# Kernel optimization log

Hardware: AMD Instinct MI355X
Metric: run time of the kernel (lower is better)

The kernel has to match this reference:

```python
import jax, jax.numpy as jnp
import numpy as np

H = 16       # query heads
KV = 4       # key/value heads
HD = 256     # head dim
ROPE_THETA = 10000.0
EPS = 1e-6


def _rms_norm(x, w):
    # Gemma RMSNorm over last dim: x / rms * (1 + w), computed in fp32
    xf = x.astype(jnp.float32)
    var = jnp.mean(xf * xf, axis=-1, keepdims=True)
    out = xf * jax.lax.rsqrt(var + EPS) * (1.0 + w.astype(jnp.float32))
    return out.astype(x.dtype)


def _rope_cos_sin(position_ids):
    # cos/sin tables of shape [S, HD]
    inv_freq = 1.0 / (ROPE_THETA ** (jnp.arange(0, HD, 2, dtype=jnp.float32) / HD))
    ang = position_ids.astype(jnp.float32)[:, None] * inv_freq[None, :]  # [S, HD/2]
    emb = jnp.concatenate([ang, ang], axis=-1)                           # [S, HD]
    return jnp.cos(emb), jnp.sin(emb)


def _rotate_half(x):
    x1, x2 = jnp.split(x, 2, axis=-1)
    return jnp.concatenate([-x2, x1], axis=-1)


def _apply_rope(x, cos, sin):
    # x: [B, h, S, HD]; cos/sin: [S, HD] -> broadcast over batch and heads
    c = cos[None, None, :, :]
    s = sin[None, None, :, :]
    return (x * c + _rotate_half(x) * s).astype(x.dtype)


def setup_inputs() -> dict:
    key = jax.random.key(0)
    ks = jax.random.split(key, 8)
    B, S, D = 2, 2048, 2048
    inp = {
        "hidden_states": jax.random.normal(ks[0], (B, S, D), jnp.float32),
        "Wq": jax.random.normal(ks[1], (D, H * HD), jnp.float32) * 0.02,
        "Wk": jax.random.normal(ks[2], (D, KV * HD), jnp.float32) * 0.02,
        "Wv": jax.random.normal(ks[3], (D, KV * HD), jnp.float32) * 0.02,
        "Wo": jax.random.normal(ks[4], (H * HD, D), jnp.float32) * 0.02,
        "q_norm_w": jnp.zeros((HD,), jnp.float32),
        "k_norm_w": jnp.zeros((HD,), jnp.float32),
        "position_ids": jnp.arange(S, dtype=jnp.int32),
    }
    return inp


def reference(hidden_states, Wq, Wk, Wv, Wo, q_norm_w, k_norm_w, position_ids):
    B, S, D = hidden_states.shape
    scale = HD ** -0.5

    # projections -> [B, h, S, HD]
    q = jnp.einsum("bsd,de->bse", hidden_states, Wq).reshape(B, S, H, HD).transpose(0, 2, 1, 3)
    k = jnp.einsum("bsd,de->bse", hidden_states, Wk).reshape(B, S, KV, HD).transpose(0, 2, 1, 3)
    v = jnp.einsum("bsd,de->bse", hidden_states, Wv).reshape(B, S, KV, HD).transpose(0, 2, 1, 3)

    # Gemma per-head RMSNorm on q/k
    q = _rms_norm(q, q_norm_w)
    k = _rms_norm(k, k_norm_w)

    # RoPE
    cos, sin = _rope_cos_sin(position_ids)
    q = _apply_rope(q, cos, sin)
    k = _apply_rope(k, cos, sin)

    # GQA: repeat kv heads to match query heads
    rep = H // KV
    k = jnp.repeat(k, rep, axis=1)  # [B, H, S, HD]
    v = jnp.repeat(v, rep, axis=1)

    # SDPA with causal mask, softmax in fp32
    scores = jnp.einsum("bhqd,bhkd->bhqk", q, k) * scale
    causal = jnp.tril(jnp.ones((S, S), dtype=bool))
    scores = jnp.where(causal[None, None, :, :], scores, jnp.finfo(jnp.float32).min)
    probs = jax.nn.softmax(scores.astype(jnp.float32), axis=-1).astype(q.dtype)
    attn = jnp.einsum("bhqk,bhkd->bhqd", probs, v)  # [B, H, S, HD]

    attn = attn.transpose(0, 2, 1, 3).reshape(B, S, H * HD)
    return jnp.einsum("bse,ed->bsd", attn, Wo)
```

## Files before the change

kernel.cpp:

```cpp
#include <hip/hip_runtime.h>

typedef unsigned short ushort_t;
typedef __bf16 bf16_t;
typedef bf16_t bf16x8 __attribute__((ext_vector_type(8)));
typedef float floatx4 __attribute__((ext_vector_type(4)));
typedef ushort_t ushort4v __attribute__((ext_vector_type(4)));
typedef ushort_t ushort8v __attribute__((ext_vector_type(8)));

static constexpr int B = 2, S = 2048, D = 2048;
static constexpr int H = 16, KVH = 4, HD = 256;

#define DEVFN static __device__ __forceinline__

DEVFN ushort_t f2b(float f) {
  union { float f; unsigned u; } x; x.f = f;
  unsigned r = x.u + 0x7fffu + ((x.u >> 16) & 1u);
  return (ushort_t)(r >> 16);
}
DEVFN float b2f(ushort_t h) {
  union { unsigned u; float f; } x; x.u = ((unsigned)h) << 16;
  return x.f;
}
DEVFN void gll16(const void* g, void* l) {
  __builtin_amdgcn_global_load_lds(
      (const __attribute__((address_space(1))) void*)g,
      (__attribute__((address_space(3))) void*)l, 16, 0, 0);
}

DEVFN void bar() {
  asm volatile("" ::: "memory");
  __builtin_amdgcn_s_barrier();
  asm volatile("" ::: "memory");
}
template <int N>
DEVFN void waitvm() { asm volatile("s_waitcnt vmcnt(%0)" ::"n"(N) : "memory"); }

DEVFN ushort4v norm_rope_row(ushort4v raw, const float* __restrict__ w,
                             const float* __restrict__ tab, int s, float scale, int lane) {
  float v[4];
  float ss = 0.f;
#pragma unroll
  for (int i = 0; i < 4; i++) { v[i] = b2f(raw[i]); ss += v[i] * v[i]; }
#pragma unroll
  for (int m = 1; m < 64; m <<= 1) ss += __shfl_xor(ss, m, 64);
  const float inv = rsqrtf(ss * (1.0f / HD) + 1e-6f);
  float4 wv = *(const float4*)(w + lane * 4);
  float y[4];
  y[0] = v[0] * inv * (1.0f + wv.x);
  y[1] = v[1] * inv * (1.0f + wv.y);
  y[2] = v[2] * inv * (1.0f + wv.z);
  y[3] = v[3] * inv * (1.0f + wv.w);
  float py[4];
#pragma unroll
  for (int i = 0; i < 4; i++) py[i] = __shfl_xor(y[i], 32, 64);
  const bool lo = (lane < 32);
  ushort4v ov;
#pragma unroll
  for (int i = 0; i < 4; i++) {
    int dd = (lane * 4 + i) & 127;
    float2 cs = *(const float2*)(tab + ((size_t)s * 128 + dd) * 2);
    float rot = lo ? -py[i] : py[i];
    ov[i] = f2b((y[i] * cs.x + rot * cs.y) * scale);
  }
  return ov;
}

__global__ void k_cvt_bf16(const float* __restrict__ in, ushort_t* __restrict__ out, int n) {
  int i = (blockIdx.x * 256 + threadIdx.x) * 4;
  if (i >= n) return;
  float4 v = *(const float4*)(in + i);
  ushort4v o;
  o[0] = f2b(v.x); o[1] = f2b(v.y); o[2] = f2b(v.z); o[3] = f2b(v.w);
  *(ushort4v*)(out + i) = o;
}

__global__ void k_transpose_cvt(const float* __restrict__ in, ushort_t* __restrict__ out,
                                int R, int C) {
  __shared__ float tile[64][65];
  const int cb = blockIdx.x * 64, rb = blockIdx.y * 64;
  const int t = threadIdx.x;
  const int l16 = t & 15, g16 = t >> 4;
#pragma unroll
  for (int p = 0; p < 4; p++) {
    const int r = p * 16 + g16;
    float4 v = *(const float4*)(in + (size_t)(rb + r) * C + cb + l16 * 4);
    tile[r][l16 * 4 + 0] = v.x;
    tile[r][l16 * 4 + 1] = v.y;
    tile[r][l16 * 4 + 2] = v.z;
    tile[r][l16 * 4 + 3] = v.w;
  }
  __syncthreads();
#pragma unroll
  for (int p = 0; p < 4; p++) {
    const int c = p * 16 + g16;
    ushort4v o4;
#pragma unroll
    for (int i = 0; i < 4; i++) o4[i] = f2b(tile[l16 * 4 + i][c]);
    *(ushort4v*)(out + (size_t)(cb + c) * R + rb + l16 * 4) = o4;
  }
}

__global__ void k_rope_table(const int* __restrict__ pos_ids, float* __restrict__ tab) {
  int idx = blockIdx.x * 256 + threadIdx.x;
  int s = idx >> 7, dd = idx & 127;
  float ang = (float)pos_ids[s] * exp2f((float)dd * (-13.287712379549449f / 128.0f));
  tab[idx * 2] = cosf(ang);
  tab[idx * 2 + 1] = sinf(ang);
}


DEVFN void stage_tile(const ushort_t* __restrict__ A, const ushort_t* __restrict__ Bt,
                      ushort_t* smb, size_t arow0, size_t brow0, int K, int kt) {
  const int t = threadIdx.x;
  const int rq = t >> 2;
  const int cq = (t & 3) * 8;
#pragma unroll
  for (int i = 0; i < 2; i++) {
    const int cs = cq ^ ((rq & 8) << 1);
    gll16(A + (arow0 + rq) * (size_t)K + kt + i * 32 + cs, smb + i * 4096 + t * 8);
  }
#pragma unroll
  for (int i = 0; i < 4; i++) {
    const int row = ((i & 1) << 7) | rq;
    const int cs = cq ^ ((row & 8) << 1);
    gll16(Bt + (brow0 + row) * (size_t)K + kt + (i >> 1) * 32 + cs,
          smb + 8192 + i * 4096 + t * 8);
  }
}

DEVFN bf16x8 ldsA(const ushort_t* buf, int row, int ks, int lq) {
  const int c = (lq * 8) ^ ((row & 8) << 1);
  return *(const bf16x8*)(buf + ks * 4096 + row * 32 + c);
}
DEVFN bf16x8 ldsB(const ushort_t* buf, int row, int ks, int lq) {
  const int c = (lq * 8) ^ ((row & 8) << 1);
  return *(const bf16x8*)(buf + 8192 + ks * 8192 + row * 32 + c);
}

template <int MODE>
__global__ __launch_bounds__(512, 2)
void k_gemm256(const ushort_t* __restrict__ A, const ushort_t* __restrict__ Bt,
               void* __restrict__ C0, void* __restrict__ C1, void* __restrict__ C2,
               int N, int K) {
  __shared__ ushort_t sm[49152];
  const int tid = threadIdx.x;
  const int lane = tid & 63, wave = tid >> 6;
  const int lr = lane & 15, lq = lane >> 4;
  const int wm = wave >> 2, wn = wave & 3;
  const size_t m0 = (size_t)blockIdx.x * 128;
  const size_t n0 = (size_t)blockIdx.y * 256;

  floatx4 acc[4][4];
#pragma unroll
  for (int i = 0; i < 4; i++)
#pragma unroll
    for (int j = 0; j < 4; j++) acc[i][j] = {0.f, 0.f, 0.f, 0.f};

  const int NT = K >> 6;
  stage_tile(A, Bt, sm, m0, n0, K, 0);
  stage_tile(A, Bt, sm + 24576, m0, n0, K, 64);

  for (int t = 0; t < NT; ++t) {
    ushort_t* bA = sm + (t & 1) * 24576;
    if (t < NT - 1) waitvm<6>(); else waitvm<0>();
    bar();

    bf16x8 a[2][4], bfr[2][4];
#pragma unroll
    for (int ks = 0; ks < 2; ks++) {
#pragma unroll
      for (int m = 0; m < 4; m++) a[ks][m] = ldsA(bA, wm * 64 + m * 16 + lr, ks, lq);
#pragma unroll
      for (int n = 0; n < 4; n++) bfr[ks][n] = ldsB(bA, wn * 64 + n * 16 + lr, ks, lq);
    }
    __builtin_amdgcn_s_setprio(1);
#pragma unroll
    for (int m = 0; m < 4; m++)
#pragma unroll
      for (int n = 0; n < 4; n++)
        acc[m][n] = __builtin_amdgcn_mfma_f32_16x16x32_bf16(a[0][m], bfr[0][n], acc[m][n], 0, 0, 0);
    __builtin_amdgcn_s_setprio(0);
    asm volatile("s_waitcnt lgkmcnt(0)" ::: "memory");
    __builtin_amdgcn_sched_barrier(0);
    bar();
    if (t + 2 < NT) stage_tile(A, Bt, bA, m0, n0, K, (t + 2) * 64);
    __builtin_amdgcn_sched_barrier(0);
    __builtin_amdgcn_s_setprio(1);
#pragma unroll
    for (int m = 0; m < 4; m++)
#pragma unroll
      for (int n = 0; n < 4; n++)
        acc[m][n] = __builtin_amdgcn_mfma_f32_16x16x32_bf16(a[1][m], bfr[1][n], acc[m][n], 0, 0, 0);
    __builtin_amdgcn_s_setprio(0);
  }

  const int colb = (int)n0;
#pragma unroll
  for (int mg = 0; mg < 4; mg++)
#pragma unroll
    for (int ng = 0; ng < 4; ng++) {
      const size_t row0 = m0 + wm * 64 + mg * 16 + lq * 4;
      const int col = colb + wn * 64 + ng * 16 + lr;
      if (MODE == 1) {
#pragma unroll
        for (int r = 0; r < 4; r++)
          ((float*)C0)[(row0 + r) * N + col] = acc[mg][ng][r];
      } else {
        if (colb < 4096) {
#pragma unroll
          for (int r = 0; r < 4; r++)
            ((ushort_t*)C0)[(row0 + r) * 4096 + col] = f2b(acc[mg][ng][r]);
        } else if (colb < 5120) {
#pragma unroll
          for (int r = 0; r < 4; r++)
            ((ushort_t*)C1)[(row0 + r) * 1024 + (col - 4096)] = f2b(acc[mg][ng][r]);
        } else {
          const int ch = col - 5120;
          const int kvh = ch >> 8, chh = ch & 255, f = chh >> 4, lrv = chh & 15;
          const size_t bb = row0 >> 11;
          const int s0 = (int)(row0 & 2047);
          const int tile = s0 >> 6, kh = (s0 >> 5) & 1, lqv = (s0 >> 3) & 3, j0 = s0 & 7;
          ushort4v pk;
#pragma unroll
          for (int r = 0; r < 4; r++) pk[r] = f2b(acc[mg][ng][r]);
          *(ushort4v*)&((ushort_t*)C2)[((bb * KVH + kvh) * (S / 64) + tile) * 16384 +
                                       (size_t)(f * 2 + kh) * 512 +
                                       (size_t)(lqv * 16 + lrv) * 8 + j0] = pk;
        }
      }
    }
}

__global__ void k_norm_rope(ushort_t* __restrict__ x, const float* __restrict__ w,
                            const float* __restrict__ tab, int heads, float scale) {
  const int lane = threadIdx.x & 63;
  const size_t row = (size_t)blockIdx.x * 4 + (threadIdx.x >> 6);
  const int s = (int)((row / heads) % S);
  ushort_t* p = x + row * HD + lane * 4;
  ushort4v raw = *(const ushort4v*)p;
  *(ushort4v*)p = norm_rope_row(raw, w, tab, s, scale, lane);
}

__global__ void k_norm_rope_k(const ushort_t* __restrict__ Kb, ushort_t* __restrict__ Kf,
                              const float* __restrict__ w, const float* __restrict__ tab) {
  __shared__ ushort_t t[64 * 264];
  const int lane = threadIdx.x & 63, wave = threadIdx.x >> 6;
  const int tile = blockIdx.x, kvh = blockIdx.y, b = blockIdx.z;
#pragma unroll
  for (int rr = 0; rr < 16; rr++) {
    const int row = wave * 16 + rr;
    const int s = tile * 64 + row;
    const ushort_t* p = Kb + ((size_t)(b * S + s) * KVH + kvh) * HD + lane * 4;
    ushort4v raw = *(const ushort4v*)p;
    *(ushort4v*)&t[row * 264 + lane * 4] = norm_rope_row(raw, w, tab, s, 1.0f, lane);
  }
  __syncthreads();
  ushort_t* dst = Kf + ((size_t)(b * KVH + kvh) * (S / 64) + tile) * 16384;
  const int lr = lane & 15, lq = lane >> 4;
#pragma unroll
  for (int q = 0; q < 8; q++) {
    const int c = wave * 8 + q;
    const int nt = c >> 3, ks = c & 7;
    ushort8v v = *(const ushort8v*)&t[(nt * 16 + lr) * 264 + ks * 32 + lq * 8];
    *(ushort8v*)&dst[(size_t)c * 512 + lane * 8] = v;
  }
}

__global__ __launch_bounds__(256, 2)
void k_attn(const ushort_t* __restrict__ Q, const ushort_t* __restrict__ Kf,
            const ushort_t* __restrict__ Vf, ushort_t* __restrict__ O) {
  __shared__ ushort_t Ks[32 * 512];
  __shared__ ushort_t Vs[32 * 512];
  __shared__ ushort_t Ps[4][16 * 72];
  const int lane = threadIdx.x & 63, wave = threadIdx.x >> 6;
  const int lr = lane & 15, lq = lane >> 4;
  const int h = blockIdx.y, b = blockIdx.z;
  const int kvh = h >> 2;
  const size_t kvb = (size_t)(b * KVH + kvh) * (S / 64);

#pragma unroll 1
  for (int half = 0; half < 2; half++) {
    const int qt = half ? (int)blockIdx.x : (S / 64 - 1 - (int)blockIdx.x);
    const int q0 = qt * 64 + wave * 16;

    bf16x8 qf[8];
    {
      const ushort_t* qp = Q + ((size_t)(b * S + q0 + lr) * H + h) * HD + lq * 8;
#pragma unroll
      for (int ks = 0; ks < 8; ks++) qf[ks] = *(const bf16x8*)(qp + ks * 32);
    }
    floatx4 o[16];
#pragma unroll
    for (int f = 0; f < 16; f++) o[f] = {0.f, 0.f, 0.f, 0.f};
    float m_i[4] = {-1e30f, -1e30f, -1e30f, -1e30f};
    float l_i[4] = {0.f, 0.f, 0.f, 0.f};

    const int ntiles = qt + 1;
    for (int kt = 0; kt < ntiles; kt++) {
      const int kbase = kt * 64;
      __syncthreads();
      const ushort_t* tb = Kf + (kvb + kt) * 16384;
      const ushort_t* vb = Vf + (kvb + kt) * 16384;
#pragma unroll
      for (int i = 0; i < 16; i++) {
        const int c = wave * 16 + i;
        if (c < 32) gll16(tb + (size_t)c * 512 + lane * 8, &Ks[c * 512 + lane * 8]);
        else        gll16(vb + (size_t)(c - 32) * 512 + lane * 8, &Vs[(c - 32) * 512 + lane * 8]);
      }
      __syncthreads();

      const int ntmax = min(4, ((q0 + 15 - kbase) >> 4) + 1);
      floatx4 sacc[4];
#pragma unroll
      for (int nt = 0; nt < 4; nt++) {
        if (nt < ntmax) {
          sacc[nt] = {0.f, 0.f, 0.f, 0.f};
#pragma unroll
          for (int ks = 0; ks < 8; ks++) {
            bf16x8 kf = *(const bf16x8*)&Ks[(nt * 8 + ks) * 512 + lane * 8];
            sacc[nt] = __builtin_amdgcn_mfma_f32_16x16x32_bf16(qf[ks], kf, sacc[nt], 0, 0, 0);
          }
        } else {
          sacc[nt] = {-1e30f, -1e30f, -1e30f, -1e30f};
        }
      }
      if (kbase + 63 > q0) {
#pragma unroll
        for (int nt = 0; nt < 4; nt++)
          if (nt < ntmax)
#pragma unroll
            for (int r = 0; r < 4; r++)
              if (kbase + nt * 16 + lr > q0 + lq * 4 + r) sacc[nt][r] = -1e30f;
      }
      float mt[4], alpha[4], rs[4];
#pragma unroll
      for (int r = 0; r < 4; r++)
        mt[r] = fmaxf(fmaxf(sacc[0][r], sacc[1][r]), fmaxf(sacc[2][r], sacc[3][r]));
#pragma unroll
      for (int m = 1; m < 16; m <<= 1)
#pragma unroll
        for (int r = 0; r < 4; r++) mt[r] = fmaxf(mt[r], __shfl_xor(mt[r], m, 64));
#pragma unroll
      for (int r = 0; r < 4; r++) {
        float mn = fmaxf(m_i[r], mt[r]);
        alpha[r] = exp2f(m_i[r] - mn);
        m_i[r] = mn;
      }
#pragma unroll
      for (int nt = 0; nt < 4; nt++)
#pragma unroll
        for (int r = 0; r < 4; r++) sacc[nt][r] = exp2f(sacc[nt][r] - m_i[r]);
#pragma unroll
      for (int r = 0; r < 4; r++)
        rs[r] = (sacc[0][r] + sacc[1][r]) + (sacc[2][r] + sacc[3][r]);
#pragma unroll
      for (int m = 1; m < 16; m <<= 1)
#pragma unroll
        for (int r = 0; r < 4; r++) rs[r] += __shfl_xor(rs[r], m, 64);
#pragma unroll
      for (int r = 0; r < 4; r++) l_i[r] = l_i[r] * alpha[r] + rs[r];
      if (__any((alpha[0] < 1.f) | (alpha[1] < 1.f) | (alpha[2] < 1.f) | (alpha[3] < 1.f))) {
#pragma unroll
        for (int f = 0; f < 16; f++) {
          o[f][0] *= alpha[0]; o[f][1] *= alpha[1];
          o[f][2] *= alpha[2]; o[f][3] *= alpha[3];
        }
      }
      ushort_t* psw = Ps[wave];
#pragma unroll
      for (int nt = 0; nt < 4; nt++)
#pragma unroll
        for (int r = 0; r < 4; r++)
          psw[(lq * 4 + r) * 72 + nt * 16 + lr] = f2b(sacc[nt][r]);
      bf16x8 pf0 = *(const bf16x8*)&psw[lr * 72 + lq * 8];
      bf16x8 pf1 = *(const bf16x8*)&psw[lr * 72 + 32 + lq * 8];
#pragma unroll
      for (int f = 0; f < 16; f++) {
        bf16x8 vf0 = *(const bf16x8*)&Vs[(f * 2 + 0) * 512 + lane * 8];
        o[f] = __builtin_amdgcn_mfma_f32_16x16x32_bf16(pf0, vf0, o[f], 0, 0, 0);
        bf16x8 vf1 = *(const bf16x8*)&Vs[(f * 2 + 1) * 512 + lane * 8];
        o[f] = __builtin_amdgcn_mfma_f32_16x16x32_bf16(pf1, vf1, o[f], 0, 0, 0);
      }
    }
    float invl[4];
#pragma unroll
    for (int r = 0; r < 4; r++) invl[r] = 1.0f / l_i[r];
#pragma unroll
    for (int f = 0; f < 16; f++)
#pragma unroll
      for (int r = 0; r < 4; r++)
        O[((size_t)(b * S + q0 + lq * 4 + r) * H + h) * HD + f * 16 + lr] =
            f2b(o[f][r] * invl[r]);
  }
}

extern "C" void kernel_launch(void* const* d_in, const int* in_sizes, int n_in,
                              void* d_out, int out_size, void* d_ws, size_t ws_size,
                              hipStream_t stream) {
  const float* hs = (const float*)d_in[0];
  const float* Wq = (const float*)d_in[1];
  const float* Wk = (const float*)d_in[2];
  const float* Wv = (const float*)d_in[3];
  const float* Wo = (const float*)d_in[4];
  const float* qw = (const float*)d_in[5];
  const float* kw = (const float*)d_in[6];
  const int* pos = (const int*)d_in[7];
  float* out = (float*)d_out;

  char* ws = (char*)d_ws;
  size_t off = 0;
  auto alloc = [&](size_t bytes) {
    void* p = ws + off;
    off += (bytes + 255) & ~(size_t)255;
    return p;
  };
  ushort_t* Xb   = (ushort_t*)alloc((size_t)B * S * D * 2);
  ushort_t* Wqt  = (ushort_t*)alloc((size_t)(H * HD) * D * 2);
  ushort_t* Wkvt = (ushort_t*)alloc((size_t)(2 * KVH * HD) * D * 2);
  ushort_t* Wot  = (ushort_t*)alloc((size_t)D * (H * HD) * 2);
  ushort_t* Qb   = (ushort_t*)alloc((size_t)B * S * H * HD * 2);
  ushort_t* Kf   = (ushort_t*)alloc((size_t)B * S * KVH * HD * 2);
  ushort_t* Vf   = (ushort_t*)alloc((size_t)B * S * KVH * HD * 2);
  ushort_t* Ab   = (ushort_t*)alloc((size_t)B * S * H * HD * 2);
  float*    tab  = (float*)alloc((size_t)S * 128 * 2 * sizeof(float));
  ushort_t* Kb = Ab;

  k_cvt_bf16<<<(B * S * D / 4 + 255) / 256, 256, 0, stream>>>(hs, Xb, B * S * D);
  k_transpose_cvt<<<dim3((H * HD) / 64, D / 64), 256, 0, stream>>>(Wq, Wqt, D, H * HD);
  k_transpose_cvt<<<dim3((KVH * HD) / 64, D / 64), 256, 0, stream>>>(Wk, Wkvt, D, KVH * HD);
  k_transpose_cvt<<<dim3((KVH * HD) / 64, D / 64), 256, 0, stream>>>(
      Wv, Wkvt + (size_t)(KVH * HD) * D, D, KVH * HD);
  k_transpose_cvt<<<dim3(D / 64, (H * HD) / 64), 256, 0, stream>>>(Wo, Wot, H * HD, D);
  k_rope_table<<<S * 128 / 256, 256, 0, stream>>>(pos, tab);

  k_gemm256<0><<<dim3((B * S) / 128, 6144 / 256), 512, 0, stream>>>(
      Xb, Wqt, Qb, Kb, Vf, 6144, D);

  k_norm_rope<<<B * S * H / 4, 256, 0, stream>>>(Qb, qw, tab, H, 0.0625f * 1.4426950408889634f);
  k_norm_rope_k<<<dim3(S / 64, KVH, B), 256, 0, stream>>>(Kb, Kf, kw, tab);

  k_attn<<<dim3(S / 128, H, B), 256, 0, stream>>>(Qb, Kf, Vf, Ab);

  k_gemm256<1><<<dim3((B * S) / 128, D / 256), 512, 0, stream>>>(
      Ab, Wot, out, nullptr, nullptr, D, H * HD);
}
```

Baseline: 509.8 us.

## Double-buffer attention K/V tiles, widen blocks to 128 queries, fuse Q norm+RoPE

The attention kernel now uses 512 threads covering 128 query rows per block. K/V tiles are double-buffered in LDS, with the next tile prefetched via global_load_lds while the current one is computed, replacing the load-then-sync pattern on every iteration. The Q RMSNorm, RoPE and softmax scaling are folded into the attention kernel's Q fragment load, so the separate k_norm_rope pass over Q is removed, and s_setprio is raised around the MFMA sections. The costs are doubled LDS use (about 146KB per block, which may limit occupancy to one block per CU despite launch_bounds(512,2)) and coarser causal load balancing with fewer blocks.

```diff
diff --git a/kernel.cpp b/kernel.cpp
--- a/kernel.cpp
+++ b/kernel.cpp
@@ -107,7 +107,6 @@
   tab[idx * 2] = cosf(ang);
   tab[idx * 2 + 1] = sinf(ang);
 }
-
 
 DEVFN void stage_tile(const ushort_t* __restrict__ A, const ushort_t* __restrict__ Bt,
                       ushort_t* smb, size_t arow0, size_t brow0, int K, int kt) {
@@ -231,16 +230,6 @@
     }
 }
 
-__global__ void k_norm_rope(ushort_t* __restrict__ x, const float* __restrict__ w,
-                            const float* __restrict__ tab, int heads, float scale) {
-  const int lane = threadIdx.x & 63;
-  const size_t row = (size_t)blockIdx.x * 4 + (threadIdx.x >> 6);
-  const int s = (int)((row / heads) % S);
-  ushort_t* p = x + row * HD + lane * 4;
-  ushort4v raw = *(const ushort4v*)p;
-  *(ushort4v*)p = norm_rope_row(raw, w, tab, s, scale, lane);
-}
-
 __global__ void k_norm_rope_k(const ushort_t* __restrict__ Kb, ushort_t* __restrict__ Kf,
                               const float* __restrict__ w, const float* __restrict__ tab) {
   __shared__ ushort_t t[64 * 264];
@@ -266,12 +255,13 @@
   }
 }
 
-__global__ __launch_bounds__(256, 2)
+__global__ __launch_bounds__(512, 2)
 void k_attn(const ushort_t* __restrict__ Q, const ushort_t* __restrict__ Kf,
-            const ushort_t* __restrict__ Vf, ushort_t* __restrict__ O) {
-  __shared__ ushort_t Ks[32 * 512];
-  __shared__ ushort_t Vs[32 * 512];
-  __shared__ ushort_t Ps[4][16 * 72];
+            const ushort_t* __restrict__ Vf, ushort_t* __restrict__ O,
+            const float* __restrict__ qw, const float* __restrict__ tab) {
+  __shared__ ushort_t Ks[2][16384];
+  __shared__ ushort_t Vs[2][16384];
+  __shared__ ushort_t Ps[8][16 * 72];
   const int lane = threadIdx.x & 63, wave = threadIdx.x >> 6;
   const int lr = lane & 15, lq = lane >> 4;
   const int h = blockIdx.y, b = blockIdx.z;
@@ -280,57 +270,107 @@
 
 #pragma unroll 1
   for (int half = 0; half < 2; half++) {
-    const int qt = half ? (int)blockIdx.x : (S / 64 - 1 - (int)blockIdx.x);
-    const int q0 = qt * 64 + wave * 16;
+    const int qt = half ? (int)blockIdx.x : (S / 128 - 1 - (int)blockIdx.x);
+    const int qw0 = qt * 128 + wave * 16;
+    const int sq = qw0 + lr;
 
     bf16x8 qf[8];
     {
-      const ushort_t* qp = Q + ((size_t)(b * S + q0 + lr) * H + h) * HD + lq * 8;
-#pragma unroll
-      for (int ks = 0; ks < 8; ks++) qf[ks] = *(const bf16x8*)(qp + ks * 32);
+      const ushort_t* qp = Q + ((size_t)(b * S + sq) * H + h) * HD + lq * 8;
+      ushort8v qr[8];
+#pragma unroll
+      for (int ks = 0; ks < 8; ks++) qr[ks] = *(const ushort8v*)(qp + ks * 32);
+      float ss = 0.f;
+#pragma unroll
+      for (int ks = 0; ks < 8; ks++)
+#pragma unroll
+        for (int j = 0; j < 8; j++) { float v = b2f(qr[ks][j]); ss += v * v; }
+      ss += __shfl_xor(ss, 16, 64);
+      ss += __shfl_xor(ss, 32, 64);
+      const float inv = rsqrtf(ss * (1.0f / HD) + 1e-6f);
+      const float sc = 0.0625f * 1.4426950408889634f;
+#pragma unroll
+      for (int c = 0; c < 4; c++) {
+        const int d0 = c * 32 + lq * 8;
+        float wl[8], wh[8];
+        {
+          float4 a0 = *(const float4*)(qw + d0);
+          float4 a1 = *(const float4*)(qw + d0 + 4);
+          float4 a2 = *(const float4*)(qw + d0 + 128);
+          float4 a3 = *(const float4*)(qw + d0 + 132);
+          wl[0]=a0.x; wl[1]=a0.y; wl[2]=a0.z; wl[3]=a0.w;
+          wl[4]=a1.x; wl[5]=a1.y; wl[6]=a1.z; wl[7]=a1.w;
+          wh[0]=a2.x; wh[1]=a2.y; wh[2]=a2.z; wh[3]=a2.w;
+          wh[4]=a3.x; wh[5]=a3.y; wh[6]=a3.z; wh[7]=a3.w;
+        }
+        const float* tp = tab + ((size_t)sq * 128 + d0) * 2;
+        ushort8v olo, ohi;
+#pragma unroll
+        for (int j = 0; j < 8; j++) {
+          float ylo = b2f(qr[c][j]) * inv * (1.0f + wl[j]);
+          float yhi = b2f(qr[c + 4][j]) * inv * (1.0f + wh[j]);
+          float2 cs = *(const float2*)(tp + j * 2);
+          olo[j] = f2b((ylo * cs.x - yhi * cs.y) * sc);
+          ohi[j] = f2b((yhi * cs.x + ylo * cs.y) * sc);
+        }
+        qf[c] = *reinterpret_cast<bf16x8*>(&olo);
+        qf[c + 4] = *reinterpret_cast<bf16x8*>(&ohi);
+      }
     }
+
     floatx4 o[16];
 #pragma unroll
     for (int f = 0; f < 16; f++) o[f] = {0.f, 0.f, 0.f, 0.f};
     float m_i[4] = {-1e30f, -1e30f, -1e30f, -1e30f};
     float l_i[4] = {0.f, 0.f, 0.f, 0.f};
 
-    const int ntiles = qt + 1;
+    const int ntiles = 2 * qt + 2;
+    {
+      const ushort_t* tb = Kf + kvb * 16384;
+      const ushort_t* vb = Vf + kvb * 16384;
+#pragma unroll
+      for (int tt = 0; tt < 2; tt++) {
+#pragma unroll
+        for (int i = 0; i < 4; i++) {
+          const int c = wave * 4 + i;
+          gll16(tb + (size_t)tt * 16384 + c * 512 + lane * 8, &Ks[tt][c * 512 + lane * 8]);
+          gll16(vb + (size_t)tt * 16384 + c * 512 + lane * 8, &Vs[tt][c * 512 + lane * 8]);
+        }
+      }
+    }
+    waitvm<8>();
+    bar();
+
     for (int kt = 0; kt < ntiles; kt++) {
       const int kbase = kt * 64;
-      __syncthreads();
-      const ushort_t* tb = Kf + (kvb + kt) * 16384;
-      const ushort_t* vb = Vf + (kvb + kt) * 16384;
-#pragma unroll
-      for (int i = 0; i < 16; i++) {
-        const int c = wave * 16 + i;
-        if (c < 32) gll16(tb + (size_t)c * 512 + lane * 8, &Ks[c * 512 + lane * 8]);
-        else        gll16(vb + (size_t)(c - 32) * 512 + lane * 8, &Vs[(c - 32) * 512 + lane * 8]);
-      }
-      __syncthreads();
-
-      const int ntmax = min(4, ((q0 + 15 - kbase) >> 4) + 1);
+      const int cur = kt & 1;
+      const ushort_t* ksb = Ks[cur];
+      const ushort_t* vsb = Vs[cur];
+
+      const int ntmax = min(4, ((qw0 + 15 - kbase) >> 4) + 1);
       floatx4 sacc[4];
+      __builtin_amdgcn_s_setprio(1);
 #pragma unroll
       for (int nt = 0; nt < 4; nt++) {
         if (nt < ntmax) {
           sacc[nt] = {0.f, 0.f, 0.f, 0.f};
 #pragma unroll
           for (int ks = 0; ks < 8; ks++) {
-            bf16x8 kf = *(const bf16x8*)&Ks[(nt * 8 + ks) * 512 + lane * 8];
+            bf16x8 kf = *(const bf16x8*)&ksb[(nt * 8 + ks) * 512 + lane * 8];
             sacc[nt] = __builtin_amdgcn_mfma_f32_16x16x32_bf16(qf[ks], kf, sacc[nt], 0, 0, 0);
           }
         } else {
           sacc[nt] = {-1e30f, -1e30f, -1e30f, -1e30f};
         }
       }
-      if (kbase + 63 > q0) {
+      __builtin_amdgcn_s_setprio(0);
+      if (kbase + 63 > qw0) {
 #pragma unroll
         for (int nt = 0; nt < 4; nt++)
           if (nt < ntmax)
 #pragma unroll
             for (int r = 0; r < 4; r++)
-              if (kbase + nt * 16 + lr > q0 + lq * 4 + r) sacc[nt][r] = -1e30f;
+              if (kbase + nt * 16 + lr > qw0 + lq * 4 + r) sacc[nt][r] = -1e30f;
       }
       float mt[4], alpha[4], rs[4];
 #pragma unroll
@@ -374,13 +414,31 @@
           psw[(lq * 4 + r) * 72 + nt * 16 + lr] = f2b(sacc[nt][r]);
       bf16x8 pf0 = *(const bf16x8*)&psw[lr * 72 + lq * 8];
       bf16x8 pf1 = *(const bf16x8*)&psw[lr * 72 + 32 + lq * 8];
+      __builtin_amdgcn_s_setprio(1);
 #pragma unroll
       for (int f = 0; f < 16; f++) {
-        bf16x8 vf0 = *(const bf16x8*)&Vs[(f * 2 + 0) * 512 + lane * 8];
+        bf16x8 vf0 = *(const bf16x8*)&vsb[(f * 2 + 0) * 512 + lane * 8];
         o[f] = __builtin_amdgcn_mfma_f32_16x16x32_bf16(pf0, vf0, o[f], 0, 0, 0);
-        bf16x8 vf1 = *(const bf16x8*)&Vs[(f * 2 + 1) * 512 + lane * 8];
+        bf16x8 vf1 = *(const bf16x8*)&vsb[(f * 2 + 1) * 512 + lane * 8];
         o[f] = __builtin_amdgcn_mfma_f32_16x16x32_bf16(pf1, vf1, o[f], 0, 0, 0);
       }
+      __builtin_amdgcn_s_setprio(0);
+
+      bar();
+      if (kt + 2 < ntiles) {
+        const ushort_t* tb = Kf + (kvb + kt + 2) * 16384;
+        const ushort_t* vb = Vf + (kvb + kt + 2) * 16384;
+#pragma unroll
+        for (int i = 0; i < 4; i++) {
+          const int c = wave * 4 + i;
+          gll16(tb + c * 512 + lane * 8, &Ks[cur][c * 512 + lane * 8]);
+          gll16(vb + c * 512 + lane * 8, &Vs[cur][c * 512 + lane * 8]);
+        }
+        waitvm<8>();
+      } else if (kt + 1 < ntiles) {
+        waitvm<0>();
+      }
+      bar();
     }
     float invl[4];
 #pragma unroll
@@ -389,7 +447,7 @@
     for (int f = 0; f < 16; f++)
 #pragma unroll
       for (int r = 0; r < 4; r++)
-        O[((size_t)(b * S + q0 + lq * 4 + r) * H + h) * HD + f * 16 + lr] =
+        O[((size_t)(b * S + qw0 + lq * 4 + r) * H + h) * HD + f * 16 + lr] =
             f2b(o[f][r] * invl[r]);
   }
 }
@@ -436,10 +494,9 @@
   k_gemm256<0><<<dim3((B * S) / 128, 6144 / 256), 512, 0, stream>>>(
       Xb, Wqt, Qb, Kb, Vf, 6144, D);
 
-  k_norm_rope<<<B * S * H / 4, 256, 0, stream>>>(Qb, qw, tab, H, 0.0625f * 1.4426950408889634f);
   k_norm_rope_k<<<dim3(S / 64, KVH, B), 256, 0, stream>>>(Kb, Kf, kw, tab);
 
-  k_attn<<<dim3(S / 128, H, B), 256, 0, stream>>>(Qb, Kf, Vf, Ab);
+  k_attn<<<dim3(S / 256, H, B), 512, 0, stream>>>(Qb, Kf, Vf, Ab, qw, tab);
 
   k_gemm256<1><<<dim3((B * S) / 128, D / 256), 512, 0, stream>>>(
       Ab, Wot, out, nullptr, nullptr, D, H * HD);
```

After: 546.2 us. 1.07x slower.
